# Performance work log

Hardware: AMD Instinct MI355X
Metric: run time of the kernel (lower is better)

Reference implementation:

```python
import jax, jax.numpy as jnp
import numpy as np

N = 8192
E = 262144
IN_SELF = 512
IN_AGG = 512
OUT = 256  # out_channels; hidden = 2*OUT = 512


def _glorot(key, shape, scale=0.05):
    return jax.random.normal(key, shape, dtype=jnp.float32) * scale


def setup_inputs() -> dict:
    key = jax.random.key(0)
    ks = jax.random.split(key, 16)
    x_self = jax.random.normal(ks[0], (N, IN_SELF), dtype=jnp.float32)
    x_neighbor = jax.random.normal(ks[1], (N, IN_AGG), dtype=jnp.float32)
    edge_index = jax.random.randint(ks[2], (2, E), 0, N, dtype=jnp.int64)
    H = 2 * OUT
    return {
        "x_self": x_self,
        "x_neighbor": x_neighbor,
        "edge_index": edge_index,
        # linear_in_self: IN_SELF -> 2*OUT
        "w_in_self": _glorot(ks[3], (IN_SELF, H)),
        "b_in_self": jnp.zeros((H,), jnp.float32),
        # linear_out_self: IN_SELF + 2*OUT -> OUT
        "w_out_self": _glorot(ks[4], (IN_SELF + H, OUT)),
        "b_out_self": jnp.zeros((OUT,), jnp.float32),
        # gcn1: IN_SELF -> 2*OUT
        "gw1": _glorot(ks[5], (IN_SELF, H)),
        "gb1": jnp.zeros((H,), jnp.float32),
        # gcn2: 2*OUT -> OUT
        "gw2": _glorot(ks[6], (H, OUT)),
        "gb2": jnp.zeros((OUT,), jnp.float32),
        # linear_out: IN_AGG + OUT -> OUT
        "w_out": _glorot(ks[7], (IN_AGG + OUT, OUT)),
        "b_out": jnp.zeros((OUT,), jnp.float32),
    }


def _gcn_norm(edge_index, n):
    # PyG GCNConv default: add self loops, symmetric deg^-1/2 normalization.
    loop = jnp.arange(n, dtype=edge_index.dtype)
    src = jnp.concatenate([edge_index[0], loop])
    dst = jnp.concatenate([edge_index[1], loop])
    deg = jax.ops.segment_sum(jnp.ones_like(dst, dtype=jnp.float32), dst, num_segments=n)
    dinv = jnp.where(deg > 0, jax.lax.rsqrt(deg), 0.0)
    norm = dinv[src] * dinv[dst]  # [E+N]
    return src, dst, norm


def _gcn(x, w, b, src, dst, norm, n):
    h = x @ w                                   # [N, out]
    msg = h[src] * norm[:, None]                # gather + scale
    agg = jax.ops.segment_sum(msg, dst, num_segments=n)
    return agg + b


def reference(x_self, x_neighbor, edge_index,
              w_in_self, b_in_self, w_out_self, b_out_self,
              gw1, gb1, gw2, gb2, w_out, b_out):
    n = x_self.shape[0]
    src, dst, norm = _gcn_norm(edge_index, n)
    # linear branch
    l1 = jax.nn.relu(x_self @ w_in_self + b_in_self)
    l1 = jnp.concatenate([x_self, l1], axis=1) @ w_out_self + b_out_self
    # GCN branch
    g1 = _gcn(x_self, gw1, gb1, src, dst, norm, n)
    g2 = _gcn(g1, gw2, gb2, src, dst, norm, n)
    x2 = jnp.concatenate([x_neighbor, g2], axis=1) @ w_out + b_out
    # concat latent, dense inner-product decode
    z = jnp.concatenate([l1, x2], axis=1)       # [N, 2*OUT]
    return jax.nn.sigmoid(z @ z.T)              # [N, N]
```

## Files before the change

### kernel.cpp

```cpp
#include <hip/hip_runtime.h>
#include <cstdint>
#include <cstddef>

#define NNODE 8192
#define NEDGE 262144

typedef __attribute__((ext_vector_type(8))) short bf16x8;
typedef __attribute__((ext_vector_type(4))) float f32x4;

__device__ __forceinline__ unsigned short f2bf_rn(float x) {
    unsigned u = __float_as_uint(x);
    u = (u + 0x7FFFu + ((u >> 16) & 1u)) >> 16;
    return (unsigned short)u;
}
__device__ __forceinline__ float bf2f(unsigned short h) {
    return __uint_as_float(((unsigned)h) << 16);
}

__device__ __forceinline__ void gload16(const char* gp, char* lp) {
    __builtin_amdgcn_global_load_lds((const __attribute__((address_space(1))) void*)gp,
                                     (__attribute__((address_space(3))) void*)lp, 16, 0, 0);
}


__global__ void k_count(const int* __restrict__ dst, int* __restrict__ cnt, int n) {
    int i = blockIdx.x * blockDim.x + threadIdx.x;
    if (i < n) atomicAdd(&cnt[dst[i]], 1);
}

__global__ __launch_bounds__(256) void k_scan(const int* __restrict__ cnt,
                                              int* __restrict__ row_start,
                                              int* __restrict__ cursor,
                                              float* __restrict__ dinv) {
    __shared__ int part[256];
    const int tid = threadIdx.x;
    const int PER = NNODE / 256;
    const int base = tid * PER;
    int loc[PER];
    int sum = 0;
#pragma unroll
    for (int i = 0; i < PER; ++i) { loc[i] = cnt[base + i]; sum += loc[i]; }
    part[tid] = sum;
    __syncthreads();
    if (tid == 0) {
        int r = 0;
        for (int i = 0; i < 256; ++i) { int t = part[i]; part[i] = r; r += t; }
    }
    __syncthreads();
    int run = part[tid];
#pragma unroll
    for (int i = 0; i < PER; ++i) {
        row_start[base + i] = run;
        cursor[base + i] = run;
        dinv[base + i] = rsqrtf((float)loc[i] + 1.0f);
        run += loc[i];
    }
    if (tid == 255) row_start[NNODE] = run;
}

__global__ void k_fill_csr2(const int* __restrict__ src, const int* __restrict__ dst,
                            int* __restrict__ cursor, const float* __restrict__ dinv,
                            int* __restrict__ slist, float* __restrict__ wlist, int n) {
    int e = blockIdx.x * blockDim.x + threadIdx.x;
    if (e < n) {
        int d = dst[e];
        int s = src[e];
        int pos = atomicAdd(&cursor[d], 1);
        slist[pos] = s;
        wlist[pos] = dinv[s] * dinv[d];
    }
}

__device__ __forceinline__ void split_wt_tile(const float* __restrict__ W, int K, int N,
                                              int k0, int n0,
                                              unsigned short* __restrict__ Oh,
                                              unsigned short* __restrict__ Ol,
                                              float (*t)[33]) {
    const int c = threadIdx.x & 31, r8 = threadIdx.x >> 5;
#pragma unroll
    for (int i = 0; i < 4; ++i) {
        int r = r8 + i * 8;
        t[r][c] = W[(size_t)(k0 + r) * N + n0 + c];
    }
    __syncthreads();
#pragma unroll
    for (int i = 0; i < 4; ++i) {
        int r = r8 + i * 8;
        float x = t[c][r];
        unsigned short h = f2bf_rn(x);
        Oh[(size_t)(n0 + r) * K + k0 + c] = h;
        Ol[(size_t)(n0 + r) * K + k0 + c] = f2bf_rn(x - bf2f(h));
    }
}

__global__ __launch_bounds__(256) void k_prep(
    const float* __restrict__ x_self, const float* __restrict__ x_neighbor,
    const float* __restrict__ w_in_self, const float* __restrict__ w_out_self,
    const float* __restrict__ w_out, const float* __restrict__ gw1,
    const float* __restrict__ gw2, const float* __restrict__ gb1,
    unsigned short* __restrict__ xsh, unsigned short* __restrict__ xsl,
    unsigned short* __restrict__ xnh, unsigned short* __restrict__ xnl,
    unsigned short* __restrict__ wAt_h, unsigned short* __restrict__ wAt_l,
    unsigned short* __restrict__ wost_h, unsigned short* __restrict__ wost_l,
    unsigned short* __restrict__ wot_h, unsigned short* __restrict__ wot_l,
    float* __restrict__ bc, int* __restrict__ cnt) {
    __shared__ float t[32][33];
    const int b = blockIdx.x;
    const int tid = threadIdx.x;
    if (b < 8192) {
        const float* src = (b < 4096) ? x_self : x_neighbor;
        unsigned short* oh = (b < 4096) ? xsh : xnh;
        unsigned short* ol = (b < 4096) ? xsl : xnl;
        const int i = (b & 4095) * 256 + tid;
        float4 v = ((const float4*)src)[i];
        float x[4] = {v.x, v.y, v.z, v.w};
        unsigned short h[4], l[4];
#pragma unroll
        for (int j = 0; j < 4; ++j) {
            h[j] = f2bf_rn(x[j]);
            l[j] = f2bf_rn(x[j] - bf2f(h[j]));
        }
        ((ushort4*)oh)[i] = make_ushort4(h[0], h[1], h[2], h[3]);
        ((ushort4*)ol)[i] = make_ushort4(l[0], l[1], l[2], l[3]);
    } else if (b < 8448) {
        const int b2 = b - 8192;
        split_wt_tile(w_in_self, 512, 512, (b2 & 15) * 32, (b2 >> 4) * 32, wAt_h, wAt_l, t);
    } else if (b < 8576) {
        const int b3 = b - 8448;
        const int k0 = (b3 & 15) * 32, n0 = (b3 >> 4) * 32;
        const int nloc = tid & 31, kg = tid >> 5;
        float a[4] = {0.f, 0.f, 0.f, 0.f};
        for (int c = 0; c < 512; ++c) {
            float g2v = gw2[(size_t)c * 256 + n0 + nloc];
#pragma unroll
            for (int i = 0; i < 4; ++i)
                a[i] += gw1[(size_t)(k0 + kg * 4 + i) * 512 + c] * g2v;
        }
#pragma unroll
        for (int i = 0; i < 4; ++i) {
            unsigned short hh = f2bf_rn(a[i]);
            wAt_h[(size_t)(512 + n0 + nloc) * 512 + k0 + kg * 4 + i] = hh;
            wAt_l[(size_t)(512 + n0 + nloc) * 512 + k0 + kg * 4 + i] = f2bf_rn(a[i] - bf2f(hh));
        }
    } else if (b < 8832) {
        const int b4 = b - 8576;
        split_wt_tile(w_out_self, 1024, 256, (b4 & 31) * 32, (b4 >> 5) * 32, wost_h, wost_l, t);
    } else if (b < 9024) {
        const int b5 = b - 8832;
        split_wt_tile(w_out, 768, 256, (b5 % 24) * 32, (b5 / 24) * 32, wot_h, wot_l, t);
    } else if (b == 9024) {
        float a = 0.0f;
        for (int c = 0; c < 512; ++c) a += gb1[c] * gw2[(size_t)c * 256 + tid];
        bc[tid] = a;
    } else {
        cnt[(b - 9025) * 256 + tid] = 0;
    }
}

__device__ __forceinline__ void stage_g(char* buf,
                                        const char* aH, const char* aL, size_t strA,
                                        const char* bH, const char* bL, size_t strB,
                                        int rloc, int w) {
#pragma unroll
    for (int i = 0; i < 2; ++i) {
        const size_t r = (size_t)(rloc + i * 64);
        char* lp = buf + i * 4096 + w * 1024;
        gload16(aH + r * strA, lp);
        gload16(aL + r * strA, lp + 8192);
    }
    gload16(bH + (size_t)rloc * strB, buf + 16384 + w * 1024);
    gload16(bL + (size_t)rloc * strB, buf + 20480 + w * 1024);
}

__device__ __forceinline__ void core_2x4(const char* cur, int w, int sread, int lane,
                                         f32x4 acc[2][4]) {
    bf16x8 ah[2], al[2], bh[4], bl[4];
#pragma unroll
    for (int m = 0; m < 2; ++m) {
        const int row = w * 32 + m * 16 + (lane & 15);
        ah[m] = *(const bf16x8*)(cur + row * 64 + sread);
        al[m] = *(const bf16x8*)(cur + 8192 + row * 64 + sread);
    }
#pragma unroll
    for (int n = 0; n < 4; ++n) {
        const int row = n * 16 + (lane & 15);
        bh[n] = *(const bf16x8*)(cur + 16384 + row * 64 + sread);
        bl[n] = *(const bf16x8*)(cur + 20480 + row * 64 + sread);
    }
#pragma unroll
    for (int m = 0; m < 2; ++m)
#pragma unroll
        for (int n = 0; n < 4; ++n) {
            acc[m][n] = __builtin_amdgcn_mfma_f32_16x16x32_bf16(ah[m], bh[n], acc[m][n], 0, 0, 0);
            acc[m][n] = __builtin_amdgcn_mfma_f32_16x16x32_bf16(ah[m], bl[n], acc[m][n], 0, 0, 0);
            acc[m][n] = __builtin_amdgcn_mfma_f32_16x16x32_bf16(al[m], bh[n], acc[m][n], 0, 0, 0);
        }
}

__global__ __launch_bounds__(256) void k_gemm128_A(
    const unsigned short* __restrict__ xsh, const unsigned short* __restrict__ xsl,
    const unsigned short* __restrict__ wAt_h, const unsigned short* __restrict__ wAt_l,
    const float* __restrict__ bias,
    unsigned short* __restrict__ l1h, unsigned short* __restrict__ l1l,
    float* __restrict__ hc) {
    __shared__ __align__(16) char smem[49152];
    const int tid = threadIdx.x, lane = tid & 63, w = tid >> 6;
    const int t0 = blockIdx.x;
    const int s = (t0 & 7) * 96 + (t0 >> 3);
    const int bm = (s / 12) * 128, bn = (s % 12) * 64;
    const int rloc = w * 16 + (lane >> 2);
    const int swz_src = ((lane & 3) ^ ((lane >> 3) & 3)) * 16;
    const int sread = ((lane >> 4) ^ ((lane >> 1) & 3)) * 16;
    const char* Ah = (const char*)xsh + (size_t)bm * 1024 + swz_src;
    const char* Al = (const char*)xsl + (size_t)bm * 1024 + swz_src;
    const char* Bh = (const char*)wAt_h + (size_t)bn * 1024 + swz_src;
    const char* Bl = (const char*)wAt_l + (size_t)bn * 1024 + swz_src;

    f32x4 acc[2][4] = {};
    stage_g(smem, Ah, Al, 1024, Bh, Bl, 1024, rloc, w);
    __syncthreads();
    for (int ks = 0; ks < 16; ++ks) {
        char* cur = smem + (ks & 1) * 24576;
        if (ks < 15) {
            const int kb = (ks + 1) * 64;
            stage_g(smem + ((ks + 1) & 1) * 24576, Ah + kb, Al + kb, 1024,
                    Bh + kb, Bl + kb, 1024, rloc, w);
        }
        core_2x4(cur, w, sread, lane, acc);
        __syncthreads();
    }

    const int rj = (lane >> 4) * 4, cc = lane & 15;
#pragma unroll
    for (int m = 0; m < 2; ++m) {
#pragma unroll
        for (int n = 0; n < 4; ++n) {
            const int col = bn + n * 16 + cc;
#pragma unroll
            for (int j = 0; j < 4; ++j) {
                const int row = bm + w * 32 + m * 16 + rj + j;
                float x = acc[m][n][j];
                if (col < 512) {
                    x += bias[col];
                    x = fmaxf(x, 0.0f);
                    unsigned short h = f2bf_rn(x);
                    l1h[(size_t)row * 512 + col] = h;
                    l1l[(size_t)row * 512 + col] = f2bf_rn(x - bf2f(h));
                } else {
                    hc[(size_t)row * 256 + (col - 512)] = x;
                }
            }
        }
    }
}

__global__ __launch_bounds__(256) void k_gemm128_Z(
    const unsigned short* __restrict__ xsh, const unsigned short* __restrict__ xsl,
    const unsigned short* __restrict__ l1h, const unsigned short* __restrict__ l1l,
    const unsigned short* __restrict__ xnh, const unsigned short* __restrict__ xnl,
    const unsigned short* __restrict__ g2h, const unsigned short* __restrict__ g2l,
    const unsigned short* __restrict__ wost_h, const unsigned short* __restrict__ wost_l,
    const unsigned short* __restrict__ wot_h, const unsigned short* __restrict__ wot_l,
    const float* __restrict__ b_out_self, const float* __restrict__ b_out,
    unsigned short* __restrict__ zhi, unsigned short* __restrict__ zlo) {
    __shared__ __align__(16) char smem[49152];
    const int t0 = blockIdx.x;
    const int s = (t0 & 7) * 64 + (t0 >> 3);
    const int half = s >> 8;
    const int rem = s & 255;
    const int bn = (rem & 3) * 64;
    const int bm = (rem >> 2) * 128;
    const int tid = threadIdx.x, lane = tid & 63, w = tid >> 6;
    const int rloc = w * 16 + (lane >> 2);
    const int swz_src = ((lane & 3) ^ ((lane >> 3) & 3)) * 16;
    const int sread = ((lane >> 4) ^ ((lane >> 1) & 3)) * 16;

    const unsigned short *A1h, *A1l, *A2h, *A2l, *Wh, *Wl;
    const float* bias;
    int Ktot;
    size_t strA2, strB;
    if (half == 0) {
        A1h = xsh; A1l = xsl; A2h = l1h; A2l = l1l; strA2 = 1024;
        Wh = wost_h; Wl = wost_l; strB = 2048; Ktot = 1024; bias = b_out_self;
    } else {
        A1h = xnh; A1l = xnl; A2h = g2h; A2l = g2l; strA2 = 512;
        Wh = wot_h; Wl = wot_l; strB = 1536; Ktot = 768; bias = b_out;
    }
    const int nsteps = Ktot / 32;
    const char* Bh = (const char*)Wh + (size_t)bn * strB + swz_src;
    const char* Bl = (const char*)Wl + (size_t)bn * strB + swz_src;

    auto asrc = [&](int k0, const char*& sh, const char*& sl, size_t& st) {
        if (k0 < 512) {
            sh = (const char*)A1h + (size_t)bm * 1024 + (size_t)k0 * 2 + swz_src;
            sl = (const char*)A1l + (size_t)bm * 1024 + (size_t)k0 * 2 + swz_src;
            st = 1024;
        } else {
            sh = (const char*)A2h + (size_t)bm * strA2 + (size_t)(k0 - 512) * 2 + swz_src;
            sl = (const char*)A2l + (size_t)bm * strA2 + (size_t)(k0 - 512) * 2 + swz_src;
            st = strA2;
        }
    };

    f32x4 acc[2][4] = {};
    {
        const char *sh, *sl; size_t st;
        asrc(0, sh, sl, st);
        stage_g(smem, sh, sl, st, Bh, Bl, strB, rloc, w);
    }
    __syncthreads();
    for (int ks = 0; ks < nsteps; ++ks) {
        char* cur = smem + (ks & 1) * 24576;
        if (ks + 1 < nsteps) {
            const char *sh, *sl; size_t st;
            asrc((ks + 1) * 32, sh, sl, st);
            stage_g(smem + ((ks + 1) & 1) * 24576, sh, sl, st,
                    Bh + (size_t)(ks + 1) * 64, Bl + (size_t)(ks + 1) * 64, strB, rloc, w);
        }
        core_2x4(cur, w, sread, lane, acc);
        __syncthreads();
    }

    const int rj = (lane >> 4) * 4, cc = lane & 15;
    const int zoff = half * 256;
#pragma unroll
    for (int m = 0; m < 2; ++m) {
#pragma unroll
        for (int n = 0; n < 4; ++n) {
            const int col = bn + n * 16 + cc;
            const float bv = bias[col];
#pragma unroll
            for (int j = 0; j < 4; ++j) {
                const int row = bm + w * 32 + m * 16 + rj + j;
                float x = acc[m][n][j] + bv;
                unsigned short h = f2bf_rn(x);
                zhi[(size_t)row * 512 + zoff + col] = h;
                zlo[(size_t)row * 512 + zoff + col] = f2bf_rn(x - bf2f(h));
            }
        }
    }
}

template <int MODE>
__global__ __launch_bounds__(256) void k_agg2(
    const int* __restrict__ row_start, const int* __restrict__ slist,
    const float* __restrict__ wlist, const float* __restrict__ dinv,
    const float* __restrict__ h,
    const float* __restrict__ bc, const float* __restrict__ b2,
    float* __restrict__ outf,
    unsigned short* __restrict__ oh, unsigned short* __restrict__ ol) {
    const int n = blockIdx.x;
    const int c = threadIdx.x;
    const float di = dinv[n];
    float acc = di * di * h[(size_t)n * 256 + c];
    float sv = di * di;
    const int e0 = row_start[n], e1 = row_start[n + 1];
    int j = e0;
    for (; j + 8 <= e1; j += 8) {
        int ss[8];
        float ww[8], vv[8];
#pragma unroll
        for (int u = 0; u < 8; ++u) { ss[u] = slist[j + u]; ww[u] = wlist[j + u]; }
#pragma unroll
        for (int u = 0; u < 8; ++u) vv[u] = h[(size_t)ss[u] * 256 + c];
#pragma unroll
        for (int u = 0; u < 8; ++u) {
            acc += ww[u] * vv[u];
            if (MODE) sv += ww[u];
        }
    }
    for (; j < e1; ++j) {
        const float wv = wlist[j];
        acc += wv * h[(size_t)slist[j] * 256 + c];
        if (MODE) sv += wv;
    }
    if (MODE == 0) {
        outf[(size_t)n * 256 + c] = acc;
    } else {
        float x = acc + sv * bc[c] + b2[c];
        unsigned short hb = f2bf_rn(x);
        oh[(size_t)n * 256 + c] = hb;
        ol[(size_t)n * 256 + c] = f2bf_rn(x - bf2f(hb));
    }
}

__device__ __forceinline__ void zzt_stage(char* buf, const char* s0, const char* s1,
                                          const char* s2, const char* s3,
                                          int rloc, int swz_src, int w, int kbyte) {
    const char* srcs[4] = {s0, s1, s2, s3};
#pragma unroll
    for (int tile = 0; tile < 4; ++tile) {
#pragma unroll
        for (int i = 0; i < 2; ++i) {
            const char* gp = srcs[tile] + (size_t)(rloc + i * 64) * 1024 + kbyte + swz_src;
            char* lp = buf + tile * 8192 + i * 4096 + w * 1024;
            gload16(gp, lp);
        }
    }
}

__global__ __launch_bounds__(256) void k_zzt_mfma(const unsigned short* __restrict__ zhi,
                                                  const unsigned short* __restrict__ zlo,
                                                  float* __restrict__ out) {
    __shared__ __align__(16) char smem[65536];
    const int tid = threadIdx.x;
    const int lane = tid & 63;
    const int w = tid >> 6;
    const int wr = w >> 1, wc = w & 1;

    const int t0 = blockIdx.x;
    const int t = (t0 & 7) * 260 + (t0 >> 3);
    int bi = (int)((sqrtf(8.0f * (float)t + 1.0f) - 1.0f) * 0.5f);
    while ((bi + 1) * (bi + 2) / 2 <= t) ++bi;
    while (bi * (bi + 1) / 2 > t) --bi;
    const int bj = t - bi * (bi + 1) / 2;

    const char* s0 = (const char*)zhi + (size_t)(bi * 128) * 1024;
    const char* s1 = (const char*)zlo + (size_t)(bi * 128) * 1024;
    const char* s2 = (const char*)zhi + (size_t)(bj * 128) * 1024;
    const char* s3 = (const char*)zlo + (size_t)(bj * 128) * 1024;

    const int rloc = w * 16 + (lane >> 2);
    const int swz_src = ((lane & 3) ^ ((lane >> 3) & 3)) * 16;
    const int sread = ((lane >> 4) ^ ((lane >> 1) & 3)) * 16;

    f32x4 acc[4][4] = {};

    zzt_stage(smem, s0, s1, s2, s3, rloc, swz_src, w, 0);
    __syncthreads();

    for (int ks = 0; ks < 16; ++ks) {
        char* cur = smem + (ks & 1) * 32768;
        if (ks < 15)
            zzt_stage(smem + ((ks + 1) & 1) * 32768, s0, s1, s2, s3, rloc, swz_src, w,
                      (ks + 1) * 64);

        bf16x8 ah[4], al[4], bh[4], bl[4];
        const char* pa = cur + (wr * 64 + (lane & 15)) * 64 + sread;
        const char* pb = cur + 16384 + (wc * 64 + (lane & 15)) * 64 + sread;
#pragma unroll
        for (int m = 0; m < 4; ++m) {
            ah[m] = *(const bf16x8*)(pa + m * 1024);
            al[m] = *(const bf16x8*)(pa + 8192 + m * 1024);
        }
#pragma unroll
        for (int n = 0; n < 4; ++n) {
            bh[n] = *(const bf16x8*)(pb + n * 1024);
            bl[n] = *(const bf16x8*)(pb + 8192 + n * 1024);
        }
#pragma unroll
        for (int m = 0; m < 4; ++m)
#pragma unroll
            for (int n = 0; n < 4; ++n) {
                acc[m][n] = __builtin_amdgcn_mfma_f32_16x16x32_bf16(ah[m], bh[n], acc[m][n], 0, 0, 0);
                acc[m][n] = __builtin_amdgcn_mfma_f32_16x16x32_bf16(ah[m], bl[n], acc[m][n], 0, 0, 0);
                acc[m][n] = __builtin_amdgcn_mfma_f32_16x16x32_bf16(al[m], bh[n], acc[m][n], 0, 0, 0);
            }
        __syncthreads();
    }

    const int rj = (lane >> 4) * 4;
    const int cc = lane & 15;
#pragma unroll
    for (int m = 0; m < 4; ++m) {
#pragma unroll
        for (int n = 0; n < 4; ++n) {
            float s[4];
#pragma unroll
            for (int j = 0; j < 4; ++j)
                s[j] = 1.0f / (1.0f + __expf(-acc[m][n][j]));
            const int gr0 = bi * 128 + wr * 64 + m * 16 + rj;
            const int gc  = bj * 128 + wc * 64 + n * 16 + cc;
#pragma unroll
            for (int j = 0; j < 4; ++j)
                __builtin_nontemporal_store(s[j], out + (size_t)(gr0 + j) * NNODE + gc);
            if (bi != bj) {
                const int mr = bj * 128 + wc * 64 + n * 16 + cc;
                const int mc = bi * 128 + wr * 64 + m * 16 + rj;
                f32x4 v = {s[0], s[1], s[2], s[3]};
                __builtin_nontemporal_store(v, (f32x4*)(out + (size_t)mr * NNODE + mc));
            }
        }
    }
}

extern "C" void kernel_launch(void* const* d_in, const int* in_sizes, int n_in,
                              void* d_out, int out_size, void* d_ws, size_t ws_size,
                              hipStream_t stream) {
    const float* x_self     = (const float*)d_in[0];
    const float* x_neighbor = (const float*)d_in[1];
    const int*   ei         = (const int*)d_in[2];
    const float* w_in_self  = (const float*)d_in[3];
    const float* b_in_self  = (const float*)d_in[4];
    const float* w_out_self = (const float*)d_in[5];
    const float* b_out_self = (const float*)d_in[6];
    const float* gw1        = (const float*)d_in[7];
    const float* gb1        = (const float*)d_in[8];
    const float* gw2        = (const float*)d_in[9];
    const float* gb2        = (const float*)d_in[10];
    const float* w_out      = (const float*)d_in[11];
    const float* b_out      = (const float*)d_in[12];
    float* out = (float*)d_out;

    char* ws = (char*)d_ws;
    const size_t MB = 1024 * 1024;
    const size_t KB = 1024;
    int*   cnt       = (int*)(ws + 0);
    int*   row_start = (int*)(ws + 32 * KB);
    int*   cursor    = (int*)(ws + 96 * KB);
    float* dinv      = (float*)(ws + 128 * KB);
    float* bc        = (float*)(ws + 192 * KB);
    int*   slist     = (int*)(ws + 2 * MB);
    float* wlist     = (float*)(ws + 3 * MB);
    unsigned short* xsh = (unsigned short*)(ws + 4 * MB);
    unsigned short* xsl = (unsigned short*)(ws + 12 * MB);
    unsigned short* xnh = (unsigned short*)(ws + 20 * MB);
    unsigned short* xnl = (unsigned short*)(ws + 28 * MB);
    unsigned short* l1h = (unsigned short*)(ws + 36 * MB);
    unsigned short* l1l = (unsigned short*)(ws + 44 * MB);
    float*          hc  = (float*)(ws + 52 * MB);
    float*          t1  = (float*)(ws + 60 * MB);
    unsigned short* g2h = (unsigned short*)(ws + 68 * MB);
    unsigned short* g2l = (unsigned short*)(ws + 72 * MB);
    unsigned short* zhi = (unsigned short*)(ws + 76 * MB);
    unsigned short* zlo = (unsigned short*)(ws + 84 * MB);
    unsigned short* wAt_h = (unsigned short*)(ws + 92 * MB);
    unsigned short* wAt_l = (unsigned short*)(ws + 93 * MB);
    unsigned short* wost_h = (unsigned short*)(ws + 94 * MB);
    unsigned short* wost_l = (unsigned short*)(ws + 95 * MB);
    unsigned short* wot_h  = (unsigned short*)(ws + 96 * MB);
    unsigned short* wot_l  = (unsigned short*)(ws + 97 * MB);

    const int* srcA = ei;
    const int* dstA = ei + NEDGE;

    k_prep<<<9057, 256, 0, stream>>>(x_self, x_neighbor, w_in_self, w_out_self, w_out,
                                     gw1, gw2, gb1, xsh, xsl, xnh, xnl,
                                     wAt_h, wAt_l, wost_h, wost_l, wot_h, wot_l, bc, cnt);

    k_count<<<NEDGE / 256, 256, 0, stream>>>(dstA, cnt, NEDGE);
    k_scan<<<1, 256, 0, stream>>>(cnt, row_start, cursor, dinv);
    k_fill_csr2<<<NEDGE / 256, 256, 0, stream>>>(srcA, dstA, cursor, dinv, slist, wlist, NEDGE);

    k_gemm128_A<<<768, 256, 0, stream>>>(
        xsh, xsl, wAt_h, wAt_l, b_in_self, l1h, l1l, hc);

    k_agg2<0><<<NNODE, 256, 0, stream>>>(row_start, slist, wlist, dinv, hc,
                                         nullptr, nullptr, t1, nullptr, nullptr);
    k_agg2<1><<<NNODE, 256, 0, stream>>>(row_start, slist, wlist, dinv, t1,
                                         bc, gb2, nullptr, g2h, g2l);

    k_gemm128_Z<<<512, 256, 0, stream>>>(
        xsh, xsl, l1h, l1l, xnh, xnl, g2h, g2l,
        wost_h, wost_l, wot_h, wot_l, b_out_self, b_out, zhi, zlo);

    k_zzt_mfma<<<2080, 256, 0, stream>>>(zhi, zlo, out);
}
```

Before: 376.3 us.

## Prefetch two K-steps ahead with explicit vmcnt waits in GEMM kernels

Restructures the double-buffered K loops of the three GEMM kernels so that two stages are in flight. The next-next tile is issued right after compute, and the loop waits with a partial s_waitcnt vmcnt instead of a full __syncthreads drain. This is meant to hide global-to-LDS load latency behind MFMA work. The zz^T kernel also raises wave priority around its MFMA block. The correctness of the hardcoded vmcnt counts depends on how many loads each stage issues, which adds fragility.

After: 371.5 us. Within noise of the previous version (-1.3%).

```diff
diff --git a/kernel.cpp b/kernel.cpp
--- a/kernel.cpp
+++ b/kernel.cpp
@@ -217,17 +217,21 @@
     const char* Bl = (const char*)wAt_l + (size_t)bn * 1024 + swz_src;
 
     f32x4 acc[2][4] = {};
-    stage_g(smem, Ah, Al, 1024, Bh, Bl, 1024, rloc, w);
-    __syncthreads();
+    stage_g(smem,         Ah,      Al,      1024, Bh,      Bl,      1024, rloc, w);
+    stage_g(smem + 24576, Ah + 64, Al + 64, 1024, Bh + 64, Bl + 64, 1024, rloc, w);
     for (int ks = 0; ks < 16; ++ks) {
-        char* cur = smem + (ks & 1) * 24576;
-        if (ks < 15) {
-            const int kb = (ks + 1) * 64;
-            stage_g(smem + ((ks + 1) & 1) * 24576, Ah + kb, Al + kb, 1024,
+        if (ks < 15) asm volatile("s_waitcnt vmcnt(6)" ::: "memory");
+        else         asm volatile("s_waitcnt vmcnt(0)" ::: "memory");
+        __builtin_amdgcn_s_barrier();
+        __builtin_amdgcn_sched_barrier(0);
+        core_2x4(smem + (ks & 1) * 24576, w, sread, lane, acc);
+        __builtin_amdgcn_sched_barrier(0);
+        __builtin_amdgcn_s_barrier();
+        if (ks < 14) {
+            const int kb = (ks + 2) * 64;
+            stage_g(smem + (ks & 1) * 24576, Ah + kb, Al + kb, 1024,
                     Bh + kb, Bl + kb, 1024, rloc, w);
         }
-        core_2x4(cur, w, sread, lane, acc);
-        __syncthreads();
     }
 
     const int rj = (lane >> 4) * 4, cc = lane & 15;
@@ -307,18 +311,23 @@
         const char *sh, *sl; size_t st;
         asrc(0, sh, sl, st);
         stage_g(smem, sh, sl, st, Bh, Bl, strB, rloc, w);
-    }
-    __syncthreads();
+        asrc(32, sh, sl, st);
+        stage_g(smem + 24576, sh, sl, st, Bh + 64, Bl + 64, strB, rloc, w);
+    }
     for (int ks = 0; ks < nsteps; ++ks) {
-        char* cur = smem + (ks & 1) * 24576;
-        if (ks + 1 < nsteps) {
+        if (ks < nsteps - 1) asm volatile("s_waitcnt vmcnt(6)" ::: "memory");
+        else                 asm volatile("s_waitcnt vmcnt(0)" ::: "memory");
+        __builtin_amdgcn_s_barrier();
+        __builtin_amdgcn_sched_barrier(0);
+        core_2x4(smem + (ks & 1) * 24576, w, sread, lane, acc);
+        __builtin_amdgcn_sched_barrier(0);
+        __builtin_amdgcn_s_barrier();
+        if (ks + 2 < nsteps) {
             const char *sh, *sl; size_t st;
-            asrc((ks + 1) * 32, sh, sl, st);
-            stage_g(smem + ((ks + 1) & 1) * 24576, sh, sl, st,
-                    Bh + (size_t)(ks + 1) * 64, Bl + (size_t)(ks + 1) * 64, strB, rloc, w);
-        }
-        core_2x4(cur, w, sread, lane, acc);
-        __syncthreads();
+            asrc((ks + 2) * 32, sh, sl, st);
+            stage_g(smem + (ks & 1) * 24576, sh, sl, st,
+                    Bh + (size_t)(ks + 2) * 64, Bl + (size_t)(ks + 2) * 64, strB, rloc, w);
+        }
     }
 
     const int rj = (lane >> 4) * 4, cc = lane & 15;
@@ -426,14 +435,15 @@
 
     f32x4 acc[4][4] = {};
 
-    zzt_stage(smem, s0, s1, s2, s3, rloc, swz_src, w, 0);
-    __syncthreads();
+    zzt_stage(smem,         s0, s1, s2, s3, rloc, swz_src, w, 0);
+    zzt_stage(smem + 32768, s0, s1, s2, s3, rloc, swz_src, w, 64);
 
     for (int ks = 0; ks < 16; ++ks) {
-        char* cur = smem + (ks & 1) * 32768;
-        if (ks < 15)
-            zzt_stage(smem + ((ks + 1) & 1) * 32768, s0, s1, s2, s3, rloc, swz_src, w,
-                      (ks + 1) * 64);
+        if (ks < 15) asm volatile("s_waitcnt vmcnt(8)" ::: "memory");
+        else         asm volatile("s_waitcnt vmcnt(0)" ::: "memory");
+        __builtin_amdgcn_s_barrier();
+        __builtin_amdgcn_sched_barrier(0);
+        const char* cur = smem + (ks & 1) * 32768;
 
         bf16x8 ah[4], al[4], bh[4], bl[4];
         const char* pa = cur + (wr * 64 + (lane & 15)) * 64 + sread;
@@ -448,6 +458,7 @@
             bh[n] = *(const bf16x8*)(pb + n * 1024);
             bl[n] = *(const bf16x8*)(pb + 8192 + n * 1024);
         }
+        __builtin_amdgcn_s_setprio(1);
 #pragma unroll
         for (int m = 0; m < 4; ++m)
 #pragma unroll
@@ -456,7 +467,12 @@
                 acc[m][n] = __builtin_amdgcn_mfma_f32_16x16x32_bf16(ah[m], bl[n], acc[m][n], 0, 0, 0);
                 acc[m][n] = __builtin_amdgcn_mfma_f32_16x16x32_bf16(al[m], bh[n], acc[m][n], 0, 0, 0);
             }
-        __syncthreads();
+        __builtin_amdgcn_s_setprio(0);
+        __builtin_amdgcn_sched_barrier(0);
+        __builtin_amdgcn_s_barrier();
+        if (ks < 14)
+            zzt_stage(smem + (ks & 1) * 32768, s0, s1, s2, s3, rloc, swz_src, w,
+                      (ks + 2) * 64);
     }
 
     const int rj = (lane >> 4) * 4;
```
